# Optimization experiments

Measured on AMD Instinct MI355X. Metric: run time of the kernel, lower is better.

The kernel has to match this reference:

```python
import jax, jax.numpy as jnp
import numpy as np

B, N, IN, HID, OUT, H = 8, 1024, 64, 64, 64, 4


def dense_gat(x, adj, W, a_src, a_dst, bias, heads):
    # x: [B,N,Fin], adj: [B,N,N] (0/1, self-loops already set), W: [heads*C, Fin]
    b, n, _ = x.shape
    c = W.shape[0] // heads
    h = (x @ W.T).reshape(b, n, heads, c)                      # [B,N,H,C]
    s = jnp.einsum('bnhc,hc->bnh', h, a_src)                   # source scores
    d = jnp.einsum('bnhc,hc->bnh', h, a_dst)                   # dest scores
    # alpha[b,i,j,h] = s[b,j,h] + d[b,i,h]
    alpha = s[:, None, :, :] + d[:, :, None, :]                # [B,N,N,H]
    alpha = jax.nn.leaky_relu(alpha, 0.2)
    alpha = jnp.where(adj[..., None] > 0, alpha, jnp.float32(-1e9))
    alpha = jax.nn.softmax(alpha, axis=2)                      # softmax over neighbors j
    out = jnp.einsum('bijh,bjhc->bihc', alpha, h)              # [B,N,H,C]
    return out.reshape(b, n, heads * c) + bias


def setup_inputs() -> dict:
    key = jax.random.key(0)
    ks = jax.random.split(key, 24)
    rn = lambda k, shape: (jax.random.normal(k, shape, jnp.float32) * 0.05)
    node_features = jax.random.normal(ks[0], (B, N, IN), jnp.float32)
    adj = jax.random.randint(ks[1], (B, N, N), 0, 2, jnp.int32)
    d = dict(
        node_features=node_features, adj=adj,
        w1=rn(ks[2], (H * HID, IN)),  as1=rn(ks[3], (H, HID)), ad1=rn(ks[4], (H, HID)), b1=rn(ks[5], (H * HID,)),
        w2=rn(ks[6], (H * HID, H * HID)), as2=rn(ks[7], (H, HID)), ad2=rn(ks[8], (H, HID)), b2=rn(ks[9], (H * HID,)),
        w3=rn(ks[10], (OUT, H * HID)), as3=rn(ks[11], (1, OUT)), ad3=rn(ks[12], (1, OUT)), b3=rn(ks[13], (OUT,)),
        wn=rn(ks[14], (OUT, OUT)), bn=rn(ks[15], (OUT,)),
        wg=rn(ks[16], (OUT, OUT)), bg=rn(ks[17], (OUT,)),
        wv=rn(ks[18], (1, 2 * OUT)), bv=rn(ks[19], (1,)),
    )
    return d


def reference(node_features, adj, w1, as1, ad1, b1, w2, as2, ad2, b2,
              w3, as3, ad3, b3, wn, bn, wg, bg, wv, bv):
    n = node_features.shape[1]
    adj_sl = jnp.maximum(adj, jnp.eye(n, dtype=adj.dtype)[None])  # add self-loops
    x = jax.nn.relu(dense_gat(node_features, adj_sl, w1, as1, ad1, b1, H))
    x = jax.nn.relu(dense_gat(x, adj_sl, w2, as2, ad2, b2, H))
    x = jax.nn.relu(dense_gat(x, adj_sl, w3, as3, ad3, b3, 1))     # [B,N,OUT]
    g = jnp.broadcast_to(x.sum(axis=-2, keepdims=True), x.shape)   # [B,N,OUT]
    h = jnp.concatenate([x @ wn.T + bn, g @ wg.T + bg], axis=-1)   # [B,N,2*OUT]
    h = jax.nn.relu(h)
    return (h @ wv.T + bv).squeeze(-1)                             # [B,N]
```

## Files before the change

kernel.cpp:

```cpp
#include <hip/hip_runtime.h>
#include <stdint.h>

#define NB 8
#define NN 1024
#define LOG2E 1.44269504088896f

typedef short short8 __attribute__((ext_vector_type(8)));
typedef float floatx4 __attribute__((ext_vector_type(4)));

static __device__ __forceinline__ short f2bf(float x) {
    union { float f; uint32_t u; } v; v.f = x;
    uint32_t r = (v.u + 0x7fffu + ((v.u >> 16) & 1u)) >> 16;
    return (short)r;
}

__global__ __launch_bounds__(256) void prep_all(const int* __restrict__ adj,
        uint64_t* __restrict__ am,
        const float* __restrict__ x0, const float* __restrict__ w1,
        const float* __restrict__ w2, const float* __restrict__ w3,
        const float* __restrict__ wn,
        ushort* __restrict__ x0b, ushort* __restrict__ wb1,
        ushort* __restrict__ wb2, ushort* __restrict__ wb3,
        ushort* __restrict__ wnb, float* __restrict__ gsum) {
    if (blockIdx.x < 2048) {
        int wave = blockIdx.x * 4 + (threadIdx.x >> 6);
        int lane = threadIdx.x & 63;
        int b = wave >> 10;
        int i = wave & 1023;
        const int* row = adj + ((size_t)b * NN + i) * NN;
        uint64_t* outp = am + ((size_t)b * NN + i) * 16;
        for (int it = 0; it < 16; ++it) {
            int j = it * 64 + lane;
            int v = (row[j] > 0) || (j == i);
            uint64_t m = __ballot(v);
            if (lane == 0) outp[it] = m;
        }
        return;
    }
    int idx = (blockIdx.x - 2048) * 256 + threadIdx.x;
    const float* src; ushort* dst; int li;
    if (idx < 131072)      { src = x0; dst = x0b; li = idx; }
    else if (idx < 135168) { src = w1; dst = wb1; li = idx - 131072; }
    else if (idx < 151552) { src = w2; dst = wb2; li = idx - 135168; }
    else if (idx < 155648) { src = w3; dst = wb3; li = idx - 151552; }
    else if (idx < 156672) { src = wn; dst = wnb; li = idx - 155648; }
    else if (idx < 156800) {
        ((float4*)gsum)[idx - 156672] = make_float4(0.f, 0.f, 0.f, 0.f);
        return;
    } else return;
    float4 v = ((const float4*)src)[li];
    ushort4 o;
    o.x = (ushort)f2bf(v.x); o.y = (ushort)f2bf(v.y);
    o.z = (ushort)f2bf(v.z); o.w = (ushort)f2bf(v.w);
    ((ushort4*)dst)[li] = o;
}

template<int K>
__global__ __launch_bounds__(256, 4) void gemm_mfma(const ushort* __restrict__ X,
        const ushort* __restrict__ Wt, ushort* __restrict__ hbT,
        const float* __restrict__ asrc, const float* __restrict__ adst,
        float* __restrict__ s_t, float* __restrict__ d_t, int nheads) {
    __shared__ ushort smem[2][64][88];
    int m0 = blockIdx.x * 64, n0 = blockIdx.y * 64;
    int hd = blockIdx.y;
    int tid = threadIdx.x, w = tid >> 6, L = tid & 63;
    int m15 = L & 15, kq = L >> 4;
    floatx4 acc[4];
#pragma unroll
    for (int ct = 0; ct < 4; ++ct) acc[ct] = (floatx4){0.f, 0.f, 0.f, 0.f};

    for (int k0 = 0; k0 < K; k0 += 64) {
#pragma unroll
        for (int it = 0; it < 2; ++it) {
            int idx = tid + it * 256;
            int r = idx >> 3, sg = idx & 7;
            *(uint4*)&smem[0][r][sg * 8] = *(const uint4*)&X[(size_t)(m0 + r) * K + k0 + sg * 8];
            *(uint4*)&smem[1][r][sg * 8] = *(const uint4*)&Wt[(size_t)(n0 + r) * K + k0 + sg * 8];
        }
        __syncthreads();
#pragma unroll
        for (int ks = 0; ks < 2; ++ks) {
            short8 a = *(const short8*)&smem[0][16 * w + m15][ks * 32 + kq * 8];
#pragma unroll
            for (int ct = 0; ct < 4; ++ct) {
                short8 bfr = *(const short8*)&smem[1][ct * 16 + m15][ks * 32 + kq * 8];
                acc[ct] = __builtin_amdgcn_mfma_f32_16x16x32_bf16(a, bfr, acc[ct], 0, 0, 0);
            }
        }
        __syncthreads();
    }

    float asv[4], adv[4];
#pragma unroll
    for (int ct = 0; ct < 4; ++ct) {
        asv[ct] = asrc[hd * 64 + ct * 16 + m15];
        adv[ct] = adst[hd * 64 + ct * 16 + m15];
    }
#pragma unroll
    for (int r = 0; r < 4; ++r) {
        float sp = acc[0][r] * asv[0] + acc[1][r] * asv[1] + acc[2][r] * asv[2] + acc[3][r] * asv[3];
        float dp = acc[0][r] * adv[0] + acc[1][r] * adv[1] + acc[2][r] * adv[2] + acc[3][r] * adv[3];
#pragma unroll
        for (int off = 1; off < 16; off <<= 1) {
            sp += __shfl_xor(sp, off);
            dp += __shfl_xor(dp, off);
        }
        if (m15 == 0) {
            int mg = m0 + 16 * w + kq * 4 + r;
            int bb = mg >> 10, node = mg & 1023;
            s_t[((size_t)(bb * nheads + hd)) * NN + node] = sp;
            d_t[((size_t)(bb * nheads + hd)) * NN + node] = dp;
        }
    }

    ushort* tb = (ushort*)smem;
#pragma unroll
    for (int ct = 0; ct < 4; ++ct)
#pragma unroll
        for (int r = 0; r < 4; ++r)
            tb[(ct * 16 + m15) * 80 + 16 * w + kq * 4 + r] = (ushort)f2bf(acc[ct][r]);
    __syncthreads();
    int bb = m0 >> 10, node0 = m0 & 1023;
    size_t base = ((size_t)(bb * nheads + hd) * 64) * NN + node0;
    int c = tid >> 2, s2 = (tid & 3) * 2;
#pragma unroll
    for (int e = 0; e < 2; ++e) {
        int sg = s2 + e;
        *(uint4*)&hbT[base + (size_t)c * NN + sg * 8] = *(const uint4*)&tb[c * 80 + sg * 8];
    }
}

__global__ __launch_bounds__(256, 4) void gat_agg_mfma(
        const ushort* __restrict__ hbT, const uint64_t* __restrict__ am,
        const float* __restrict__ s_t, const float* __restrict__ d_t,
        const float* __restrict__ bias, ushort* __restrict__ Xb,
        float* __restrict__ gsum, int nheads, int do_colsum) {
    __shared__ float s_lds[NN];
    __shared__ float red4[4];
    __shared__ ushort buf[4][4096];

    int i0 = blockIdx.x * 16;
    int hd = blockIdx.y;
    int b  = blockIdx.z;
    int HC = nheads * 64;
    int tid = threadIdx.x, w = tid >> 6, L = tid & 63;
    int m15 = L & 15, kq = L >> 4;

    const float* srow = s_t + ((size_t)b * nheads + hd) * NN;
    float4 s4 = ((const float4*)srow)[tid];
    *(float4*)&s_lds[tid * 4] = s4;
    float lm = fmaxf(fmaxf(s4.x, s4.y), fmaxf(s4.z, s4.w));
#pragma unroll
    for (int off = 32; off; off >>= 1) lm = fmaxf(lm, __shfl_xor(lm, off));
    if (L == 0) red4[w] = lm;

    const uint64_t* amrow = am + ((size_t)b * NN + i0 + m15) * 16 + w * 4;
    uint64_t aw[4];
    *(uint4*)&aw[0] = *(const uint4*)&amrow[0];
    *(uint4*)&aw[2] = *(const uint4*)&amrow[2];
    float d_i = d_t[((size_t)b * nheads + hd) * NN + i0 + m15];
    __syncthreads();

    float smax = fmaxf(fmaxf(red4[0], red4[1]), fmaxf(red4[2], red4[3]));
    float t0 = smax + d_i;
    float m_up = fmaxf(t0, 0.2f * t0);
    float m2n = -m_up * LOG2E;

    floatx4 acc[4];
#pragma unroll
    for (int ct = 0; ct < 4; ++ct) acc[ct] = (floatx4){0.f, 0.f, 0.f, 0.f};
    float lsum = 0.f;

    const ushort* hbase = hbT + ((size_t)(b * nheads + hd) * 64) * NN;
    int r8 = L >> 3, sl = L & 7;
    int wofs = r8 * 64 + ((sl ^ r8) * 8);
    ushort* mybuf = buf[w];
    const ushort* gsrc = hbase + (size_t)r8 * NN + (w * 4) * 64 + sl * 8;

    uint4 pre[8];
#pragma unroll
    for (int e = 0; e < 8; ++e) pre[e] = *(const uint4*)(gsrc + (size_t)e * 8 * NN);

#pragma unroll
    for (int t = 0; t < 4; ++t) {
        int jc = w * 4 + t;
#pragma unroll
        for (int e = 0; e < 8; ++e) *(uint4*)&mybuf[wofs + e * 512] = pre[e];
        if (t < 3) {
#pragma unroll
            for (int e = 0; e < 8; ++e)
                pre[e] = *(const uint4*)(gsrc + (size_t)e * 8 * NN + (t + 1) * 64);
        }
        uint64_t word = aw[t];
#pragma unroll
        for (int ks = 0; ks < 2; ++ks) {
            int jb = jc * 64 + ks * 32 + kq * 8;
            float sv[8];
            *(float4*)&sv[0] = *(const float4*)&s_lds[jb];
            *(float4*)&sv[4] = *(const float4*)&s_lds[jb + 4];
            unsigned byte = (unsigned)((word >> (ks * 32 + kq * 8)) & 0xffull);
            unsigned ue[8];
#pragma unroll
            for (int u = 0; u < 8; ++u) {
                float sc = sv[u] + d_i;
                float lk = fmaxf(sc, 0.2f * sc);
#if __has_builtin(__builtin_amdgcn_exp2f)
                float arg = __builtin_fmaf(lk, LOG2E, m2n);
                arg = ((byte >> u) & 1u) ? arg : -1e30f;
                float e = __builtin_amdgcn_exp2f(arg);
#else
                float e = __expf(lk - m_up);
                e = ((byte >> u) & 1u) ? e : 0.f;
#endif
                lsum += e;
                ue[u] = __float_as_uint(e);
            }
            unsigned pk[4];
#pragma unroll
            for (int k2 = 0; k2 < 4; ++k2)
#if __has_builtin(__builtin_amdgcn_perm)
                pk[k2] = __builtin_amdgcn_perm(ue[2 * k2 + 1], ue[2 * k2], 0x07060302u);
#else
                pk[k2] = (ue[2 * k2] >> 16) | (ue[2 * k2 + 1] & 0xffff0000u);
#endif
            short8 afrag;
            *(uint4*)&afrag = *(uint4*)&pk[0];
            int pslot = (ks * 4 + kq) ^ (m15 & 7);
#pragma unroll
            for (int ct = 0; ct < 4; ++ct) {
                short8 bfr = *(const short8*)&mybuf[(ct * 16 + m15) * 64 + pslot * 8];
                acc[ct] = __builtin_amdgcn_mfma_f32_16x16x32_bf16(afrag, bfr, acc[ct], 0, 0, 0);
            }
        }
    }

    lsum += __shfl_xor(lsum, 16);
    lsum += __shfl_xor(lsum, 32);

    float* fb = (float*)&buf[w][0];
#pragma unroll
    for (int ct = 0; ct < 4; ++ct)
#pragma unroll
        for (int r = 0; r < 4; ++r)
            fb[(kq * 4 + r) * 68 + ct * 16 + m15] = acc[ct][r];
    if (kq == 0) fb[16 * 68 + m15] = lsum;
    __syncthreads();

    int rr = tid >> 4, c0 = (tid & 15) * 4;
    float s0 = 0.f, s1 = 0.f, s2 = 0.f, s3 = 0.f, ltot = 0.f;
#pragma unroll
    for (int w2 = 0; w2 < 4; ++w2) {
        const float* f2 = (const float*)&buf[w2][0];
        float4 a4 = *(const float4*)&f2[rr * 68 + c0];
        s0 += a4.x; s1 += a4.y; s2 += a4.z; s3 += a4.w;
        ltot += f2[16 * 68 + rr];
    }
    float li = 1.f / ltot;
    float4 bv = *(const float4*)&bias[hd * 64 + c0];
    float v0 = fmaxf(s0 * li + bv.x, 0.f);
    float v1 = fmaxf(s1 * li + bv.y, 0.f);
    float v2 = fmaxf(s2 * li + bv.z, 0.f);
    float v3 = fmaxf(s3 * li + bv.w, 0.f);
    ushort4 o;
    o.x = (ushort)f2bf(v0); o.y = (ushort)f2bf(v1);
    o.z = (ushort)f2bf(v2); o.w = (ushort)f2bf(v3);
    *(ushort4*)&Xb[((size_t)(b * NN + i0 + rr)) * HC + hd * 64 + c0] = o;

    if (do_colsum) {
        __syncthreads();
        float* cb = (float*)&buf[0][0];
        *(float4*)&cb[rr * 68 + c0] = make_float4(v0, v1, v2, v3);
        __syncthreads();
        if (tid < 64) {
            float s = 0.f;
#pragma unroll
            for (int r2 = 0; r2 < 16; ++r2) s += cb[r2 * 68 + tid];
            atomicAdd(&gsum[b * 64 + tid], s);
        }
    }
}

__global__ __launch_bounds__(256) void readout_fused(
        const ushort* __restrict__ xb, const ushort* __restrict__ wnb,
        const float* __restrict__ bn, const float* __restrict__ wg,
        const float* __restrict__ bg, const float* __restrict__ wv,
        const float* __restrict__ bv, const float* __restrict__ gsum,
        float* __restrict__ outp) {
    __shared__ ushort xs[64][88];
    __shared__ ushort wns[64][88];
    __shared__ float gcs;
    int b = blockIdx.y, n0 = blockIdx.x * 64;
    int tid = threadIdx.x, w = tid >> 6, L = tid & 63;
    int m15 = L & 15, kq = L >> 4;
#pragma unroll
    for (int it = 0; it < 2; ++it) {
        int idx = tid + it * 256;
        int r = idx >> 3, sg = idx & 7;
        *(uint4*)&xs[r][sg * 8]  = *(const uint4*)&xb[(size_t)(b * NN + n0 + r) * 64 + sg * 8];
        *(uint4*)&wns[r][sg * 8] = *(const uint4*)&wnb[r * 64 + sg * 8];
    }
    if (tid < 64) {
        float acc = bg[tid];
#pragma unroll 8
        for (int c = 0; c < 64; ++c) acc += gsum[b * 64 + c] * wg[tid * 64 + c];
        acc = fmaxf(acc, 0.f) * wv[64 + tid];
#pragma unroll
        for (int off = 32; off; off >>= 1) acc += __shfl_down(acc, off);
        if (tid == 0) gcs = acc + bv[0];
    }
    __syncthreads();

    floatx4 acc[4];
#pragma unroll
    for (int ct = 0; ct < 4; ++ct) acc[ct] = (floatx4){0.f, 0.f, 0.f, 0.f};
#pragma unroll
    for (int ks = 0; ks < 2; ++ks) {
        short8 a = *(const short8*)&xs[16 * w + m15][ks * 32 + kq * 8];
#pragma unroll
        for (int ct = 0; ct < 4; ++ct) {
            short8 bfr = *(const short8*)&wns[ct * 16 + m15][ks * 32 + kq * 8];
            acc[ct] = __builtin_amdgcn_mfma_f32_16x16x32_bf16(a, bfr, acc[ct], 0, 0, 0);
        }
    }
    float bnv[4], wvv[4];
#pragma unroll
    for (int ct = 0; ct < 4; ++ct) {
        bnv[ct] = bn[ct * 16 + m15];
        wvv[ct] = wv[ct * 16 + m15];
    }
    float gc = gcs;
#pragma unroll
    for (int r = 0; r < 4; ++r) {
        float rp = 0.f;
#pragma unroll
        for (int ct = 0; ct < 4; ++ct)
            rp += fmaxf(acc[ct][r] + bnv[ct], 0.f) * wvv[ct];
#pragma unroll
        for (int off = 1; off < 16; off <<= 1) rp += __shfl_xor(rp, off);
        if (m15 == 0)
            outp[(size_t)b * NN + n0 + 16 * w + kq * 4 + r] = rp + gc;
    }
}

extern "C" void kernel_launch(void* const* d_in, const int* in_sizes, int n_in,
                              void* d_out, int out_size, void* d_ws, size_t ws_size,
                              hipStream_t stream) {
    const float* x0  = (const float*)d_in[0];
    const int*   adj = (const int*)  d_in[1];
    const float* w1  = (const float*)d_in[2];
    const float* as1 = (const float*)d_in[3];
    const float* ad1 = (const float*)d_in[4];
    const float* b1  = (const float*)d_in[5];
    const float* w2  = (const float*)d_in[6];
    const float* as2 = (const float*)d_in[7];
    const float* ad2 = (const float*)d_in[8];
    const float* b2  = (const float*)d_in[9];
    const float* w3  = (const float*)d_in[10];
    const float* as3 = (const float*)d_in[11];
    const float* ad3 = (const float*)d_in[12];
    const float* b3  = (const float*)d_in[13];
    const float* wn  = (const float*)d_in[14];
    const float* bn  = (const float*)d_in[15];
    const float* wg  = (const float*)d_in[16];
    const float* bg  = (const float*)d_in[17];
    const float* wv  = (const float*)d_in[18];
    const float* bv  = (const float*)d_in[19];
    float* outp = (float*)d_out;

    char* wsb = (char*)d_ws;
    uint64_t* amask = (uint64_t*)(wsb);
    ushort* hbT  = (ushort*)(wsb + (1u  << 20));
    ushort* xbA  = (ushort*)(wsb + (5u  << 20));
    ushort* xbB  = (ushort*)(wsb + (9u  << 20));
    ushort* x0b  = (ushort*)(wsb + (13u << 20));
    char* tail   = wsb + (14u << 20);
    float* s_buf = (float*)(tail);
    float* d_buf = (float*)(tail + (1u << 17));
    ushort* wb1  = (ushort*)(tail + (2u << 17));
    ushort* wb2  = (ushort*)(tail + (2u << 17) + (1u << 15));
    ushort* wb3  = (ushort*)(tail + (2u << 17) + (5u << 15));
    ushort* wnb  = (ushort*)(tail + (2u << 17) + (6u << 15));
    float* gsum  = (float*) (tail + (2u << 17) + (6u << 15) + (1u << 13));

    prep_all<<<2661, 256, 0, stream>>>(adj, amask, x0, w1, w2, w3, wn,
                                       x0b, wb1, wb2, wb3, wnb, gsum);

    gemm_mfma<64><<<dim3(128, 4), 256, 0, stream>>>(x0b, wb1, hbT, as1, ad1, s_buf, d_buf, 4);
    gat_agg_mfma<<<dim3(64, 4, 8), 256, 0, stream>>>(hbT, amask, s_buf, d_buf, b1, xbA, gsum, 4, 0);

    gemm_mfma<256><<<dim3(128, 4), 256, 0, stream>>>(xbA, wb2, hbT, as2, ad2, s_buf, d_buf, 4);
    gat_agg_mfma<<<dim3(64, 4, 8), 256, 0, stream>>>(hbT, amask, s_buf, d_buf, b2, xbB, gsum, 4, 0);

    gemm_mfma<256><<<dim3(128, 1), 256, 0, stream>>>(xbB, wb3, hbT, as3, ad3, s_buf, d_buf, 1);
    gat_agg_mfma<<<dim3(64, 1, 8), 256, 0, stream>>>(hbT, amask, s_buf, d_buf, b3, xbA, gsum, 1, 1);

    readout_fused<<<dim3(16, 8), 256, 0, stream>>>(xbA, wnb, bn, wg, bg, wv, bv, gsum, outp);
}
```

Measured before the change: 183.3 us.

## Process 32 destination rows per aggregation block and load h fragments directly from global

The aggregation kernel is templated on the number of destination rows per block. With 32 rows, each loaded h fragment feeds MFMAs for two 16-row groups, which halves the grid for the 4-head layers and doubles reuse of the neighbor features. The LDS staging and prefetch of h tiles is removed, so B fragments are now read straight from global memory into registers. The cost is higher register pressure from the doubled accumulators, and the direct global loads are less coalesced and no longer prefetched ahead of use.

```diff
diff --git a/kernel.cpp b/kernel.cpp
--- a/kernel.cpp
+++ b/kernel.cpp
@@ -130,16 +130,19 @@
     }
 }
 
+template<int ROWS>
 __global__ __launch_bounds__(256, 4) void gat_agg_mfma(
         const ushort* __restrict__ hbT, const uint64_t* __restrict__ am,
         const float* __restrict__ s_t, const float* __restrict__ d_t,
         const float* __restrict__ bias, ushort* __restrict__ Xb,
         float* __restrict__ gsum, int nheads, int do_colsum) {
-    __shared__ float s_lds[NN];
+    constexpr int RG = ROWS / 16;
+    __shared__ __align__(16) float s_lds[NN];
     __shared__ float red4[4];
-    __shared__ ushort buf[4][4096];
-
-    int i0 = blockIdx.x * 16;
+    __shared__ float lden[4][RG][16];
+    __shared__ __align__(16) float fb[4][ROWS][68];
+
+    int i0 = blockIdx.x * ROWS;
     int hd = blockIdx.y;
     int b  = blockIdx.z;
     int HC = nheads * 64;
@@ -154,128 +157,153 @@
     for (int off = 32; off; off >>= 1) lm = fmaxf(lm, __shfl_xor(lm, off));
     if (L == 0) red4[w] = lm;
 
-    const uint64_t* amrow = am + ((size_t)b * NN + i0 + m15) * 16 + w * 4;
-    uint64_t aw[4];
-    *(uint4*)&aw[0] = *(const uint4*)&amrow[0];
-    *(uint4*)&aw[2] = *(const uint4*)&amrow[2];
-    float d_i = d_t[((size_t)b * nheads + hd) * NN + i0 + m15];
+    uint64_t aw[RG][4];
+    float d_i[RG];
+#pragma unroll
+    for (int rg = 0; rg < RG; ++rg) {
+        const uint64_t* amrow = am + ((size_t)b * NN + i0 + rg * 16 + m15) * 16 + w * 4;
+        *(uint4*)&aw[rg][0] = *(const uint4*)&amrow[0];
+        *(uint4*)&aw[rg][2] = *(const uint4*)&amrow[2];
+        d_i[rg] = d_t[((size_t)b * nheads + hd) * NN + i0 + rg * 16 + m15];
+    }
     __syncthreads();
 
     float smax = fmaxf(fmaxf(red4[0], red4[1]), fmaxf(red4[2], red4[3]));
-    float t0 = smax + d_i;
-    float m_up = fmaxf(t0, 0.2f * t0);
-    float m2n = -m_up * LOG2E;
-
-    floatx4 acc[4];
-#pragma unroll
-    for (int ct = 0; ct < 4; ++ct) acc[ct] = (floatx4){0.f, 0.f, 0.f, 0.f};
-    float lsum = 0.f;
-
-    const ushort* hbase = hbT + ((size_t)(b * nheads + hd) * 64) * NN;
-    int r8 = L >> 3, sl = L & 7;
-    int wofs = r8 * 64 + ((sl ^ r8) * 8);
-    ushort* mybuf = buf[w];
-    const ushort* gsrc = hbase + (size_t)r8 * NN + (w * 4) * 64 + sl * 8;
-
-    uint4 pre[8];
-#pragma unroll
-    for (int e = 0; e < 8; ++e) pre[e] = *(const uint4*)(gsrc + (size_t)e * 8 * NN);
+    float m2n[RG];
+#pragma unroll
+    for (int rg = 0; rg < RG; ++rg) {
+        float t0 = smax + d_i[rg];
+        float m_up = fmaxf(t0, 0.2f * t0);
+        m2n[rg] = -m_up * LOG2E;
+    }
+
+    floatx4 acc[4][RG];
+#pragma unroll
+    for (int ct = 0; ct < 4; ++ct)
+#pragma unroll
+        for (int rg = 0; rg < RG; ++rg) acc[ct][rg] = (floatx4){0.f, 0.f, 0.f, 0.f};
+    float lsum[RG];
+#pragma unroll
+    for (int rg = 0; rg < RG; ++rg) lsum[rg] = 0.f;
+
+    const ushort* hb = hbT + ((size_t)(b * nheads + hd) * 64) * NN;
 
 #pragma unroll
     for (int t = 0; t < 4; ++t) {
         int jc = w * 4 + t;
 #pragma unroll
-        for (int e = 0; e < 8; ++e) *(uint4*)&mybuf[wofs + e * 512] = pre[e];
-        if (t < 3) {
-#pragma unroll
-            for (int e = 0; e < 8; ++e)
-                pre[e] = *(const uint4*)(gsrc + (size_t)e * 8 * NN + (t + 1) * 64);
-        }
-        uint64_t word = aw[t];
-#pragma unroll
         for (int ks = 0; ks < 2; ++ks) {
             int jb = jc * 64 + ks * 32 + kq * 8;
+            short8 bfr[4];
+#pragma unroll
+            for (int ct = 0; ct < 4; ++ct)
+                *(uint4*)&bfr[ct] = *(const uint4*)&hb[(size_t)(ct * 16 + m15) * NN + jb];
             float sv[8];
             *(float4*)&sv[0] = *(const float4*)&s_lds[jb];
             *(float4*)&sv[4] = *(const float4*)&s_lds[jb + 4];
-            unsigned byte = (unsigned)((word >> (ks * 32 + kq * 8)) & 0xffull);
-            unsigned ue[8];
-#pragma unroll
-            for (int u = 0; u < 8; ++u) {
-                float sc = sv[u] + d_i;
-                float lk = fmaxf(sc, 0.2f * sc);
+#pragma unroll
+            for (int rg = 0; rg < RG; ++rg) {
+                unsigned byte = (unsigned)((aw[rg][t] >> (ks * 32 + kq * 8)) & 0xffull);
+                unsigned ue[8];
+#pragma unroll
+                for (int u = 0; u < 8; ++u) {
+                    float sc = sv[u] + d_i[rg];
+                    float lk = fmaxf(sc, 0.2f * sc);
 #if __has_builtin(__builtin_amdgcn_exp2f)
-                float arg = __builtin_fmaf(lk, LOG2E, m2n);
-                arg = ((byte >> u) & 1u) ? arg : -1e30f;
-                float e = __builtin_amdgcn_exp2f(arg);
+                    float arg = __builtin_fmaf(lk, LOG2E, m2n[rg]);
+                    arg = ((byte >> u) & 1u) ? arg : -1e30f;
+                    float e = __builtin_amdgcn_exp2f(arg);
 #else
-                float e = __expf(lk - m_up);
-                e = ((byte >> u) & 1u) ? e : 0.f;
+                    float e = __expf(fminf(lk + m2n[rg], 0.f));
+                    e = ((byte >> u) & 1u) ? e : 0.f;
 #endif
-                lsum += e;
-                ue[u] = __float_as_uint(e);
+                    lsum[rg] += e;
+                    ue[u] = __float_as_uint(e);
+                }
+                unsigned pk[4];
+#pragma unroll
+                for (int k2 = 0; k2 < 4; ++k2)
+#if __has_builtin(__builtin_amdgcn_perm)
+                    pk[k2] = __builtin_amdgcn_perm(ue[2 * k2 + 1], ue[2 * k2], 0x07060302u);
+#else
+                    pk[k2] = (ue[2 * k2] >> 16) | (ue[2 * k2 + 1] & 0xffff0000u);
+#endif
+                short8 afrag;
+                *(uint4*)&afrag = *(uint4*)&pk[0];
+#pragma unroll
+                for (int ct = 0; ct < 4; ++ct)
+                    acc[ct][rg] = __builtin_amdgcn_mfma_f32_16x16x32_bf16(afrag, bfr[ct], acc[ct][rg], 0, 0, 0);
             }
-            unsigned pk[4];
-#pragma unroll
-            for (int k2 = 0; k2 < 4; ++k2)
-#if __has_builtin(__builtin_amdgcn_perm)
-                pk[k2] = __builtin_amdgcn_perm(ue[2 * k2 + 1], ue[2 * k2], 0x07060302u);
-#else
-                pk[k2] = (ue[2 * k2] >> 16) | (ue[2 * k2 + 1] & 0xffff0000u);
-#endif
-            short8 afrag;
-            *(uint4*)&afrag = *(uint4*)&pk[0];
-            int pslot = (ks * 4 + kq) ^ (m15 & 7);
-#pragma unroll
-            for (int ct = 0; ct < 4; ++ct) {
-                short8 bfr = *(const short8*)&mybuf[(ct * 16 + m15) * 64 + pslot * 8];
-                acc[ct] = __builtin_amdgcn_mfma_f32_16x16x32_bf16(afrag, bfr, acc[ct], 0, 0, 0);
+        }
+    }
+
+#pragma unroll
+    for (int rg = 0; rg < RG; ++rg) {
+        lsum[rg] += __shfl_xor(lsum[rg], 16);
+        lsum[rg] += __shfl_xor(lsum[rg], 32);
+        if (kq == 0) lden[w][rg][m15] = lsum[rg];
+#pragma unroll
+        for (int ct = 0; ct < 4; ++ct)
+#pragma unroll
+            for (int r = 0; r < 4; ++r)
+                fb[w][rg * 16 + kq * 4 + r][ct * 16 + m15] = acc[ct][rg][r];
+    }
+    __syncthreads();
+
+    if (ROWS == 32) {
+        int rr = tid >> 3, c0 = (tid & 7) * 8;
+        float s0[8];
+#pragma unroll
+        for (int k2 = 0; k2 < 8; ++k2) s0[k2] = 0.f;
+        float ltot = 0.f;
+#pragma unroll
+        for (int w2 = 0; w2 < 4; ++w2) {
+            float4 a4 = *(const float4*)&fb[w2][rr][c0];
+            float4 b4 = *(const float4*)&fb[w2][rr][c0 + 4];
+            s0[0] += a4.x; s0[1] += a4.y; s0[2] += a4.z; s0[3] += a4.w;
+            s0[4] += b4.x; s0[5] += b4.y; s0[6] += b4.z; s0[7] += b4.w;
+            ltot += lden[w2][rr >> 4][rr & 15];
+        }
+        float li = 1.f / ltot;
+        float4 bv0 = *(const float4*)&bias[hd * 64 + c0];
+        float4 bv1 = *(const float4*)&bias[hd * 64 + c0 + 4];
+        float bvv[8] = {bv0.x, bv0.y, bv0.z, bv0.w, bv1.x, bv1.y, bv1.z, bv1.w};
+        ushort o[8];
+#pragma unroll
+        for (int k2 = 0; k2 < 8; ++k2) {
+            float v = fmaxf(s0[k2] * li + bvv[k2], 0.f);
+            o[k2] = (ushort)f2bf(v);
+        }
+        *(uint4*)&Xb[((size_t)(b * NN + i0 + rr)) * HC + hd * 64 + c0] = *(uint4*)&o[0];
+    } else {
+        int rr = tid >> 4, c0 = (tid & 15) * 4;
+        float s0 = 0.f, s1 = 0.f, s2 = 0.f, s3 = 0.f, ltot = 0.f;
+#pragma unroll
+        for (int w2 = 0; w2 < 4; ++w2) {
+            float4 a4 = *(const float4*)&fb[w2][rr][c0];
+            s0 += a4.x; s1 += a4.y; s2 += a4.z; s3 += a4.w;
+            ltot += lden[w2][0][rr];
+        }
+        float li = 1.f / ltot;
+        float4 bv = *(const float4*)&bias[hd * 64 + c0];
+        float v0 = fmaxf(s0 * li + bv.x, 0.f);
+        float v1 = fmaxf(s1 * li + bv.y, 0.f);
+        float v2 = fmaxf(s2 * li + bv.z, 0.f);
+        float v3 = fmaxf(s3 * li + bv.w, 0.f);
+        ushort4 o;
+        o.x = (ushort)f2bf(v0); o.y = (ushort)f2bf(v1);
+        o.z = (ushort)f2bf(v2); o.w = (ushort)f2bf(v3);
+        *(ushort4*)&Xb[((size_t)(b * NN + i0 + rr)) * HC + hd * 64 + c0] = o;
+        if (do_colsum) {
+            __syncthreads();
+            *(float4*)&fb[0][rr][c0] = make_float4(v0, v1, v2, v3);
+            __syncthreads();
+            if (tid < 64) {
+                float s = 0.f;
+#pragma unroll
+                for (int r2 = 0; r2 < 16; ++r2) s += fb[0][r2][tid];
+                atomicAdd(&gsum[b * 64 + tid], s);
             }
-        }
-    }
-
-    lsum += __shfl_xor(lsum, 16);
-    lsum += __shfl_xor(lsum, 32);
-
-    float* fb = (float*)&buf[w][0];
-#pragma unroll
-    for (int ct = 0; ct < 4; ++ct)
-#pragma unroll
-        for (int r = 0; r < 4; ++r)
-            fb[(kq * 4 + r) * 68 + ct * 16 + m15] = acc[ct][r];
-    if (kq == 0) fb[16 * 68 + m15] = lsum;
-    __syncthreads();
-
-    int rr = tid >> 4, c0 = (tid & 15) * 4;
-    float s0 = 0.f, s1 = 0.f, s2 = 0.f, s3 = 0.f, ltot = 0.f;
-#pragma unroll
-    for (int w2 = 0; w2 < 4; ++w2) {
-        const float* f2 = (const float*)&buf[w2][0];
-        float4 a4 = *(const float4*)&f2[rr * 68 + c0];
-        s0 += a4.x; s1 += a4.y; s2 += a4.z; s3 += a4.w;
-        ltot += f2[16 * 68 + rr];
-    }
-    float li = 1.f / ltot;
-    float4 bv = *(const float4*)&bias[hd * 64 + c0];
-    float v0 = fmaxf(s0 * li + bv.x, 0.f);
-    float v1 = fmaxf(s1 * li + bv.y, 0.f);
-    float v2 = fmaxf(s2 * li + bv.z, 0.f);
-    float v3 = fmaxf(s3 * li + bv.w, 0.f);
-    ushort4 o;
-    o.x = (ushort)f2bf(v0); o.y = (ushort)f2bf(v1);
-    o.z = (ushort)f2bf(v2); o.w = (ushort)f2bf(v3);
-    *(ushort4*)&Xb[((size_t)(b * NN + i0 + rr)) * HC + hd * 64 + c0] = o;
-
-    if (do_colsum) {
-        __syncthreads();
-        float* cb = (float*)&buf[0][0];
-        *(float4*)&cb[rr * 68 + c0] = make_float4(v0, v1, v2, v3);
-        __syncthreads();
-        if (tid < 64) {
-            float s = 0.f;
-#pragma unroll
-            for (int r2 = 0; r2 < 16; ++r2) s += cb[r2 * 68 + tid];
-            atomicAdd(&gsum[b * 64 + tid], s);
         }
     }
 }
@@ -386,13 +414,13 @@
                                        x0b, wb1, wb2, wb3, wnb, gsum);
 
     gemm_mfma<64><<<dim3(128, 4), 256, 0, stream>>>(x0b, wb1, hbT, as1, ad1, s_buf, d_buf, 4);
-    gat_agg_mfma<<<dim3(64, 4, 8), 256, 0, stream>>>(hbT, amask, s_buf, d_buf, b1, xbA, gsum, 4, 0);
+    gat_agg_mfma<32><<<dim3(32, 4, 8), 256, 0, stream>>>(hbT, amask, s_buf, d_buf, b1, xbA, gsum, 4, 0);
 
     gemm_mfma<256><<<dim3(128, 4), 256, 0, stream>>>(xbA, wb2, hbT, as2, ad2, s_buf, d_buf, 4);
-    gat_agg_mfma<<<dim3(64, 4, 8), 256, 0, stream>>>(hbT, amask, s_buf, d_buf, b2, xbB, gsum, 4, 0);
+    gat_agg_mfma<32><<<dim3(32, 4, 8), 256, 0, stream>>>(hbT, amask, s_buf, d_buf, b2, xbB, gsum, 4, 0);
 
     gemm_mfma<256><<<dim3(128, 1), 256, 0, stream>>>(xbB, wb3, hbT, as3, ad3, s_buf, d_buf, 1);
-    gat_agg_mfma<<<dim3(64, 1, 8), 256, 0, stream>>>(hbT, amask, s_buf, d_buf, b3, xbA, gsum, 1, 1);
+    gat_agg_mfma<16><<<dim3(64, 1, 8), 256, 0, stream>>>(hbT, amask, s_buf, d_buf, b3, xbA, gsum, 1, 1);
 
     readout_fused<<<dim3(16, 8), 256, 0, stream>>>(xbA, wnb, bn, wg, bg, wv, bv, gsum, outp);
 }
```

After: 199.4 us. +8.8%, slower.

## Fuse all GAT stages into one persistent kernel with grid barriers

Applied to the files above, without the earlier changes.

Replaces the eight separate kernel launches with a single persistent kernel that loops over tiles of each stage and separates stages with a software grid barrier built on atomics. Shared memory is unioned across the stage types. This is meant to remove launch gaps and inter-kernel drain costs, but it adds barrier spin overhead and a memset launch, and the grid size is capped by occupancy. The barrier has a timeout guard, so correctness depends on all blocks being co-resident. It also clamps the exp argument in the aggregation.

```diff
diff --git a/kernel.cpp b/kernel.cpp
--- a/kernel.cpp
+++ b/kernel.cpp
@@ -14,57 +14,49 @@
     return (short)r;
 }
 
-__global__ __launch_bounds__(256) void prep_all(const int* __restrict__ adj,
-        uint64_t* __restrict__ am,
-        const float* __restrict__ x0, const float* __restrict__ w1,
-        const float* __restrict__ w2, const float* __restrict__ w3,
-        const float* __restrict__ wn,
-        ushort* __restrict__ x0b, ushort* __restrict__ wb1,
-        ushort* __restrict__ wb2, ushort* __restrict__ wb3,
-        ushort* __restrict__ wnb, float* __restrict__ gsum) {
-    if (blockIdx.x < 2048) {
-        int wave = blockIdx.x * 4 + (threadIdx.x >> 6);
-        int lane = threadIdx.x & 63;
-        int b = wave >> 10;
-        int i = wave & 1023;
-        const int* row = adj + ((size_t)b * NN + i) * NN;
-        uint64_t* outp = am + ((size_t)b * NN + i) * 16;
-        for (int it = 0; it < 16; ++it) {
-            int j = it * 64 + lane;
-            int v = (row[j] > 0) || (j == i);
-            uint64_t m = __ballot(v);
-            if (lane == 0) outp[it] = m;
-        }
-        return;
-    }
-    int idx = (blockIdx.x - 2048) * 256 + threadIdx.x;
-    const float* src; ushort* dst; int li;
-    if (idx < 131072)      { src = x0; dst = x0b; li = idx; }
-    else if (idx < 135168) { src = w1; dst = wb1; li = idx - 131072; }
-    else if (idx < 151552) { src = w2; dst = wb2; li = idx - 135168; }
-    else if (idx < 155648) { src = w3; dst = wb3; li = idx - 151552; }
-    else if (idx < 156672) { src = wn; dst = wnb; li = idx - 155648; }
-    else if (idx < 156800) {
-        ((float4*)gsum)[idx - 156672] = make_float4(0.f, 0.f, 0.f, 0.f);
-        return;
-    } else return;
-    float4 v = ((const float4*)src)[li];
-    ushort4 o;
-    o.x = (ushort)f2bf(v.x); o.y = (ushort)f2bf(v.y);
-    o.z = (ushort)f2bf(v.z); o.w = (ushort)f2bf(v.w);
-    ((ushort4*)dst)[li] = o;
+struct SmemGemm { ushort t[2][64][88]; };
+struct SmemAgg  { float s[NN]; float red4[4]; ushort buf[4][4096]; };
+struct SmemRead { ushort xs[64][88]; ushort wns[64][88]; float gcs; };
+union SmemU { SmemGemm g; SmemAgg a; SmemRead r; };
+
+struct GArgs {
+    const int* adj;
+    const float *x0, *w1, *w2, *w3, *wn;
+    const float *as1, *ad1, *b1, *as2, *ad2, *b2, *as3, *ad3, *b3;
+    const float *bn, *wg, *bg, *wv, *bv;
+    uint64_t* amask;
+    ushort *hbT, *xbA, *xbB, *x0b, *wb1, *wb2, *wb3, *wnb;
+    float *s_buf, *d_buf, *gsum;
+    unsigned* bar;
+    float* outp;
+    int nblk;
+};
+
+static __device__ __forceinline__ void gridbar(unsigned* cnt, unsigned target) {
+    __threadfence();
+    __syncthreads();
+    if (threadIdx.x == 0) {
+        __hip_atomic_fetch_add(cnt, 1u, __ATOMIC_RELEASE, __HIP_MEMORY_SCOPE_AGENT);
+        unsigned guard = 0;
+        while (__hip_atomic_load(cnt, __ATOMIC_ACQUIRE, __HIP_MEMORY_SCOPE_AGENT) < target) {
+            __builtin_amdgcn_s_sleep(2);
+            if (++guard > (1u << 20)) break;
+        }
+    }
+    __syncthreads();
+    __threadfence();
 }
 
 template<int K>
-__global__ __launch_bounds__(256, 4) void gemm_mfma(const ushort* __restrict__ X,
+static __device__ void gemm_tile(SmemU& S, const ushort* __restrict__ X,
         const ushort* __restrict__ Wt, ushort* __restrict__ hbT,
         const float* __restrict__ asrc, const float* __restrict__ adst,
-        float* __restrict__ s_t, float* __restrict__ d_t, int nheads) {
-    __shared__ ushort smem[2][64][88];
-    int m0 = blockIdx.x * 64, n0 = blockIdx.y * 64;
-    int hd = blockIdx.y;
+        float* __restrict__ s_t, float* __restrict__ d_t, int nheads,
+        int mt, int hd) {
+    int m0 = mt * 64, n0 = hd * 64;
     int tid = threadIdx.x, w = tid >> 6, L = tid & 63;
     int m15 = L & 15, kq = L >> 4;
+    __syncthreads();
     floatx4 acc[4];
 #pragma unroll
     for (int ct = 0; ct < 4; ++ct) acc[ct] = (floatx4){0.f, 0.f, 0.f, 0.f};
@@ -74,16 +66,16 @@
         for (int it = 0; it < 2; ++it) {
             int idx = tid + it * 256;
             int r = idx >> 3, sg = idx & 7;
-            *(uint4*)&smem[0][r][sg * 8] = *(const uint4*)&X[(size_t)(m0 + r) * K + k0 + sg * 8];
-            *(uint4*)&smem[1][r][sg * 8] = *(const uint4*)&Wt[(size_t)(n0 + r) * K + k0 + sg * 8];
+            *(uint4*)&S.g.t[0][r][sg * 8] = *(const uint4*)&X[(size_t)(m0 + r) * K + k0 + sg * 8];
+            *(uint4*)&S.g.t[1][r][sg * 8] = *(const uint4*)&Wt[(size_t)(n0 + r) * K + k0 + sg * 8];
         }
         __syncthreads();
 #pragma unroll
         for (int ks = 0; ks < 2; ++ks) {
-            short8 a = *(const short8*)&smem[0][16 * w + m15][ks * 32 + kq * 8];
+            short8 a = *(const short8*)&S.g.t[0][16 * w + m15][ks * 32 + kq * 8];
 #pragma unroll
             for (int ct = 0; ct < 4; ++ct) {
-                short8 bfr = *(const short8*)&smem[1][ct * 16 + m15][ks * 32 + kq * 8];
+                short8 bfr = *(const short8*)&S.g.t[1][ct * 16 + m15][ks * 32 + kq * 8];
                 acc[ct] = __builtin_amdgcn_mfma_f32_16x16x32_bf16(a, bfr, acc[ct], 0, 0, 0);
             }
         }
@@ -113,7 +105,7 @@
         }
     }
 
-    ushort* tb = (ushort*)smem;
+    ushort* tb = (ushort*)&S.g.t[0][0][0];
 #pragma unroll
     for (int ct = 0; ct < 4; ++ct)
 #pragma unroll
@@ -130,21 +122,17 @@
     }
 }
 
-__global__ __launch_bounds__(256, 4) void gat_agg_mfma(
-        const ushort* __restrict__ hbT, const uint64_t* __restrict__ am,
-        const float* __restrict__ s_t, const float* __restrict__ d_t,
-        const float* __restrict__ bias, ushort* __restrict__ Xb,
-        float* __restrict__ gsum, int nheads, int do_colsum) {
-    __shared__ float s_lds[NN];
-    __shared__ float red4[4];
-    __shared__ ushort buf[4][4096];
-
-    int i0 = blockIdx.x * 16;
-    int hd = blockIdx.y;
-    int b  = blockIdx.z;
+static __device__ void agg_tile(SmemU& S, const ushort* __restrict__ hbT,
+        const uint64_t* __restrict__ am, const float* __restrict__ s_t,
+        const float* __restrict__ d_t, const float* __restrict__ bias,
+        ushort* __restrict__ Xb, float* __restrict__ gsum, int nheads,
+        int do_colsum, int it, int hd, int b) {
+    float* s_lds = S.a.s;
+    int i0 = it * 16;
     int HC = nheads * 64;
     int tid = threadIdx.x, w = tid >> 6, L = tid & 63;
     int m15 = L & 15, kq = L >> 4;
+    __syncthreads();
 
     const float* srow = s_t + ((size_t)b * nheads + hd) * NN;
     float4 s4 = ((const float4*)srow)[tid];
@@ -152,7 +140,7 @@
     float lm = fmaxf(fmaxf(s4.x, s4.y), fmaxf(s4.z, s4.w));
 #pragma unroll
     for (int off = 32; off; off >>= 1) lm = fmaxf(lm, __shfl_xor(lm, off));
-    if (L == 0) red4[w] = lm;
+    if (L == 0) S.a.red4[w] = lm;
 
     const uint64_t* amrow = am + ((size_t)b * NN + i0 + m15) * 16 + w * 4;
     uint64_t aw[4];
@@ -161,7 +149,7 @@
     float d_i = d_t[((size_t)b * nheads + hd) * NN + i0 + m15];
     __syncthreads();
 
-    float smax = fmaxf(fmaxf(red4[0], red4[1]), fmaxf(red4[2], red4[3]));
+    float smax = fmaxf(fmaxf(S.a.red4[0], S.a.red4[1]), fmaxf(S.a.red4[2], S.a.red4[3]));
     float t0 = smax + d_i;
     float m_up = fmaxf(t0, 0.2f * t0);
     float m2n = -m_up * LOG2E;
@@ -174,7 +162,7 @@
     const ushort* hbase = hbT + ((size_t)(b * nheads + hd) * 64) * NN;
     int r8 = L >> 3, sl = L & 7;
     int wofs = r8 * 64 + ((sl ^ r8) * 8);
-    ushort* mybuf = buf[w];
+    ushort* mybuf = S.a.buf[w];
     const ushort* gsrc = hbase + (size_t)r8 * NN + (w * 4) * 64 + sl * 8;
 
     uint4 pre[8];
@@ -209,7 +197,7 @@
                 arg = ((byte >> u) & 1u) ? arg : -1e30f;
                 float e = __builtin_amdgcn_exp2f(arg);
 #else
-                float e = __expf(lk - m_up);
+                float e = __expf(fminf(lk + m2n, 0.f));
                 e = ((byte >> u) & 1u) ? e : 0.f;
 #endif
                 lsum += e;
@@ -237,7 +225,7 @@
     lsum += __shfl_xor(lsum, 16);
     lsum += __shfl_xor(lsum, 32);
 
-    float* fb = (float*)&buf[w][0];
+    float* fb = (float*)&S.a.buf[w][0];
 #pragma unroll
     for (int ct = 0; ct < 4; ++ct)
 #pragma unroll
@@ -250,7 +238,7 @@
     float s0 = 0.f, s1 = 0.f, s2 = 0.f, s3 = 0.f, ltot = 0.f;
 #pragma unroll
     for (int w2 = 0; w2 < 4; ++w2) {
-        const float* f2 = (const float*)&buf[w2][0];
+        const float* f2 = (const float*)&S.a.buf[w2][0];
         float4 a4 = *(const float4*)&f2[rr * 68 + c0];
         s0 += a4.x; s1 += a4.y; s2 += a4.z; s3 += a4.w;
         ltot += f2[16 * 68 + rr];
@@ -268,7 +256,7 @@
 
     if (do_colsum) {
         __syncthreads();
-        float* cb = (float*)&buf[0][0];
+        float* cb = (float*)&S.a.buf[0][0];
         *(float4*)&cb[rr * 68 + c0] = make_float4(v0, v1, v2, v3);
         __syncthreads();
         if (tid < 64) {
@@ -280,24 +268,21 @@
     }
 }
 
-__global__ __launch_bounds__(256) void readout_fused(
-        const ushort* __restrict__ xb, const ushort* __restrict__ wnb,
-        const float* __restrict__ bn, const float* __restrict__ wg,
-        const float* __restrict__ bg, const float* __restrict__ wv,
-        const float* __restrict__ bv, const float* __restrict__ gsum,
-        float* __restrict__ outp) {
-    __shared__ ushort xs[64][88];
-    __shared__ ushort wns[64][88];
-    __shared__ float gcs;
-    int b = blockIdx.y, n0 = blockIdx.x * 64;
+static __device__ void readout_tile(SmemU& S, const ushort* __restrict__ xb,
+        const ushort* __restrict__ wnb, const float* __restrict__ bn,
+        const float* __restrict__ wg, const float* __restrict__ bg,
+        const float* __restrict__ wv, const float* __restrict__ bv,
+        const float* __restrict__ gsum, float* __restrict__ outp, int bx, int b) {
+    int n0 = bx * 64;
     int tid = threadIdx.x, w = tid >> 6, L = tid & 63;
     int m15 = L & 15, kq = L >> 4;
+    __syncthreads();
 #pragma unroll
     for (int it = 0; it < 2; ++it) {
         int idx = tid + it * 256;
         int r = idx >> 3, sg = idx & 7;
-        *(uint4*)&xs[r][sg * 8]  = *(const uint4*)&xb[(size_t)(b * NN + n0 + r) * 64 + sg * 8];
-        *(uint4*)&wns[r][sg * 8] = *(const uint4*)&wnb[r * 64 + sg * 8];
+        *(uint4*)&S.r.xs[r][sg * 8]  = *(const uint4*)&xb[(size_t)(b * NN + n0 + r) * 64 + sg * 8];
+        *(uint4*)&S.r.wns[r][sg * 8] = *(const uint4*)&wnb[r * 64 + sg * 8];
     }
     if (tid < 64) {
         float acc = bg[tid];
@@ -306,7 +291,7 @@
         acc = fmaxf(acc, 0.f) * wv[64 + tid];
 #pragma unroll
         for (int off = 32; off; off >>= 1) acc += __shfl_down(acc, off);
-        if (tid == 0) gcs = acc + bv[0];
+        if (tid == 0) S.r.gcs = acc + bv[0];
     }
     __syncthreads();
 
@@ -315,10 +300,10 @@
     for (int ct = 0; ct < 4; ++ct) acc[ct] = (floatx4){0.f, 0.f, 0.f, 0.f};
 #pragma unroll
     for (int ks = 0; ks < 2; ++ks) {
-        short8 a = *(const short8*)&xs[16 * w + m15][ks * 32 + kq * 8];
+        short8 a = *(const short8*)&S.r.xs[16 * w + m15][ks * 32 + kq * 8];
 #pragma unroll
         for (int ct = 0; ct < 4; ++ct) {
-            short8 bfr = *(const short8*)&wns[ct * 16 + m15][ks * 32 + kq * 8];
+            short8 bfr = *(const short8*)&S.r.wns[ct * 16 + m15][ks * 32 + kq * 8];
             acc[ct] = __builtin_amdgcn_mfma_f32_16x16x32_bf16(a, bfr, acc[ct], 0, 0, 0);
         }
     }
@@ -328,7 +313,7 @@
         bnv[ct] = bn[ct * 16 + m15];
         wvv[ct] = wv[ct * 16 + m15];
     }
-    float gc = gcs;
+    float gc = S.r.gcs;
 #pragma unroll
     for (int r = 0; r < 4; ++r) {
         float rp = 0.f;
@@ -342,57 +327,127 @@
     }
 }
 
+__global__ __launch_bounds__(256) void gat_fused(GArgs A) {
+    __shared__ SmemU S;
+    int bid = blockIdx.x, tid = threadIdx.x;
+    int nblk = A.nblk;
+    int w = tid >> 6, L = tid & 63;
+    unsigned bno = 0;
+
+    {
+        int gw = bid * 4 + w, nw = nblk * 4;
+        for (int row = gw; row < NB * NN; row += nw) {
+            int b = row >> 10, i = row & 1023;
+            const int* rp = A.adj + ((size_t)b * NN + i) * NN;
+            uint64_t* op = A.amask + ((size_t)b * NN + i) * 16;
+            for (int it = 0; it < 16; ++it) {
+                int j = it * 64 + L;
+                int v = (rp[j] > 0) || (j == i);
+                uint64_t m = __ballot(v);
+                if (L == 0) op[it] = m;
+            }
+        }
+        for (int idx = bid * 256 + tid; idx < 156800; idx += nblk * 256) {
+            if (idx < 156672) {
+                const float* src; ushort* dst; int li;
+                if (idx < 131072)      { src = A.x0; dst = A.x0b; li = idx; }
+                else if (idx < 135168) { src = A.w1; dst = A.wb1; li = idx - 131072; }
+                else if (idx < 151552) { src = A.w2; dst = A.wb2; li = idx - 135168; }
+                else if (idx < 155648) { src = A.w3; dst = A.wb3; li = idx - 151552; }
+                else                   { src = A.wn; dst = A.wnb; li = idx - 155648; }
+                float4 v = ((const float4*)src)[li];
+                ushort4 o;
+                o.x = (ushort)f2bf(v.x); o.y = (ushort)f2bf(v.y);
+                o.z = (ushort)f2bf(v.z); o.w = (ushort)f2bf(v.w);
+                ((ushort4*)dst)[li] = o;
+            } else {
+                ((float4*)A.gsum)[idx - 156672] = make_float4(0.f, 0.f, 0.f, 0.f);
+            }
+        }
+    }
+    gridbar(A.bar, ++bno * (unsigned)nblk);
+
+    for (int v = bid; v < 512; v += nblk)
+        gemm_tile<64>(S, A.x0b, A.wb1, A.hbT, A.as1, A.ad1, A.s_buf, A.d_buf, 4, v & 127, v >> 7);
+    gridbar(A.bar, ++bno * (unsigned)nblk);
+
+    for (int v = bid; v < 2048; v += nblk)
+        agg_tile(S, A.hbT, A.amask, A.s_buf, A.d_buf, A.b1, A.xbA, A.gsum, 4, 0,
+                 v & 63, (v >> 6) & 3, v >> 8);
+    gridbar(A.bar, ++bno * (unsigned)nblk);
+
+    for (int v = bid; v < 512; v += nblk)
+        gemm_tile<256>(S, A.xbA, A.wb2, A.hbT, A.as2, A.ad2, A.s_buf, A.d_buf, 4, v & 127, v >> 7);
+    gridbar(A.bar, ++bno * (unsigned)nblk);
+
+    for (int v = bid; v < 2048; v += nblk)
+        agg_tile(S, A.hbT, A.amask, A.s_buf, A.d_buf, A.b2, A.xbB, A.gsum, 4, 0,
+                 v & 63, (v >> 6) & 3, v >> 8);
+    gridbar(A.bar, ++bno * (unsigned)nblk);
+
+    for (int v = bid; v < 128; v += nblk)
+        gemm_tile<256>(S, A.xbB, A.wb3, A.hbT, A.as3, A.ad3, A.s_buf, A.d_buf, 1, v, 0);
+    gridbar(A.bar, ++bno * (unsigned)nblk);
+
+    for (int v = bid; v < 512; v += nblk)
+        agg_tile(S, A.hbT, A.amask, A.s_buf, A.d_buf, A.b3, A.xbA, A.gsum, 1, 1,
+                 v & 63, 0, v >> 6);
+    gridbar(A.bar, ++bno * (unsigned)nblk);
+
+    for (int v = bid; v < 128; v += nblk)
+        readout_tile(S, A.xbA, A.wnb, A.bn, A.wg, A.bg, A.wv, A.bv, A.gsum, A.outp,
+                     v & 15, v >> 4);
+}
+
 extern "C" void kernel_launch(void* const* d_in, const int* in_sizes, int n_in,
                               void* d_out, int out_size, void* d_ws, size_t ws_size,
                               hipStream_t stream) {
-    const float* x0  = (const float*)d_in[0];
-    const int*   adj = (const int*)  d_in[1];
-    const float* w1  = (const float*)d_in[2];
-    const float* as1 = (const float*)d_in[3];
-    const float* ad1 = (const float*)d_in[4];
-    const float* b1  = (const float*)d_in[5];
-    const float* w2  = (const float*)d_in[6];
-    const float* as2 = (const float*)d_in[7];
-    const float* ad2 = (const float*)d_in[8];
-    const float* b2  = (const float*)d_in[9];
-    const float* w3  = (const float*)d_in[10];
-    const float* as3 = (const float*)d_in[11];
-    const float* ad3 = (const float*)d_in[12];
-    const float* b3  = (const float*)d_in[13];
-    const float* wn  = (const float*)d_in[14];
-    const float* bn  = (const float*)d_in[15];
-    const float* wg  = (const float*)d_in[16];
-    const float* bg  = (const float*)d_in[17];
-    const float* wv  = (const float*)d_in[18];
-    const float* bv  = (const float*)d_in[19];
-    float* outp = (float*)d_out;
+    GArgs A;
+    A.x0  = (const float*)d_in[0];
+    A.adj = (const int*)  d_in[1];
+    A.w1  = (const float*)d_in[2];
+    A.as1 = (const float*)d_in[3];
+    A.ad1 = (const float*)d_in[4];
+    A.b1  = (const float*)d_in[5];
+    A.w2  = (const float*)d_in[6];
+    A.as2 = (const float*)d_in[7];
+    A.ad2 = (const float*)d_in[8];
+    A.b2  = (const float*)d_in[9];
+    A.w3  = (const float*)d_in[10];
+    A.as3 = (const float*)d_in[11];
+    A.ad3 = (const float*)d_in[12];
+    A.b3  = (const float*)d_in[13];
+    A.wn  = (const float*)d_in[14];
+    A.bn  = (const float*)d_in[15];
+    A.wg  = (const float*)d_in[16];
+    A.bg  = (const float*)d_in[17];
+    A.wv  = (const float*)d_in[18];
+    A.bv  = (const float*)d_in[19];
+    A.outp = (float*)d_out;
 
     char* wsb = (char*)d_ws;
-    uint64_t* amask = (uint64_t*)(wsb);
-    ushort* hbT  = (ushort*)(wsb + (1u  << 20));
-    ushort* xbA  = (ushort*)(wsb + (5u  << 20));
-    ushort* xbB  = (ushort*)(wsb + (9u  << 20));
-    ushort* x0b  = (ushort*)(wsb + (13u << 20));
-    char* tail   = wsb + (14u << 20);
-    float* s_buf = (float*)(tail);
-    float* d_buf = (float*)(tail + (1u << 17));
-    ushort* wb1  = (ushort*)(tail + (2u << 17));
-    ushort* wb2  = (ushort*)(tail + (2u << 17) + (1u << 15));
-    ushort* wb3  = (ushort*)(tail + (2u << 17) + (5u << 15));
-    ushort* wnb  = (ushort*)(tail + (2u << 17) + (6u << 15));
-    float* gsum  = (float*) (tail + (2u << 17) + (6u << 15) + (1u << 13));
-
-    prep_all<<<2661, 256, 0, stream>>>(adj, amask, x0, w1, w2, w3, wn,
-                                       x0b, wb1, wb2, wb3, wnb, gsum);
-
-    gemm_mfma<64><<<dim3(128, 4), 256, 0, stream>>>(x0b, wb1, hbT, as1, ad1, s_buf, d_buf, 4);
-    gat_agg_mfma<<<dim3(64, 4, 8), 256, 0, stream>>>(hbT, amask, s_buf, d_buf, b1, xbA, gsum, 4, 0);
-
-    gemm_mfma<256><<<dim3(128, 4), 256, 0, stream>>>(xbA, wb2, hbT, as2, ad2, s_buf, d_buf, 4);
-    gat_agg_mfma<<<dim3(64, 4, 8), 256, 0, stream>>>(hbT, amask, s_buf, d_buf, b2, xbB, gsum, 4, 0);
-
-    gemm_mfma<256><<<dim3(128, 1), 256, 0, stream>>>(xbB, wb3, hbT, as3, ad3, s_buf, d_buf, 1);
-    gat_agg_mfma<<<dim3(64, 1, 8), 256, 0, stream>>>(hbT, amask, s_buf, d_buf, b3, xbA, gsum, 1, 1);
-
-    readout_fused<<<dim3(16, 8), 256, 0, stream>>>(xbA, wnb, bn, wg, bg, wv, bv, gsum, outp);
-}
+    A.amask = (uint64_t*)(wsb);
+    A.hbT  = (ushort*)(wsb + (1u  << 20));
+    A.xbA  = (ushort*)(wsb + (5u  << 20));
+    A.xbB  = (ushort*)(wsb + (9u  << 20));
+    A.x0b  = (ushort*)(wsb + (13u << 20));
+    char* tail = wsb + (14u << 20);
+    A.s_buf = (float*)(tail);
+    A.d_buf = (float*)(tail + (1u << 17));
+    A.wb1  = (ushort*)(tail + (2u << 17));
+    A.wb2  = (ushort*)(tail + (2u << 17) + (1u << 15));
+    A.wb3  = (ushort*)(tail + (2u << 17) + (5u << 15));
+    A.wnb  = (ushort*)(tail + (2u << 17) + (6u << 15));
+    A.gsum = (float*) (tail + (2u << 17) + (6u << 15) + (1u << 13));
+    A.bar  = (unsigned*)(tail + (2u << 17) + (6u << 15) + (1u << 13) + 4096);
+
+    int nb = 0;
+    if (hipOccupancyMaxActiveBlocksPerMultiprocessor(&nb, gat_fused, 256, 0) != hipSuccess || nb < 1)
+        nb = 1;
+    int nblk = nb * 256;
+    if (nblk > 2048) nblk = 2048;
+    A.nblk = nblk;
+
+    hipMemsetAsync(A.bar, 0, 256, stream);
+    gat_fused<<<nblk, 256, 0, stream>>>(A);
+}
```

After: 661.7 us. 261% more time.
